# Optimization experiments

Measured on AMD Instinct MI355X. Metric: run time of the kernel, lower is better.

The kernel has to match this reference:

```python
import jax, jax.numpy as jnp
import numpy as np

K = 1024            # atoms per chain
L = 4 * K - 9       # 2*(K-3) sin/cos dihedrals + (K-2) len13 + (K-1) bond lengths
EPS = 1e-6


def _denorm(v, lo, hi):
    # map [-1, 1] -> [lo, hi]
    return (v + 1.0) * 0.5 * (hi - lo) + lo


def _output_arr2values(v):
    # split flat NN output into (sin/cos dihedrals, hedron len13, bond lengths)
    n_d = K - 3
    sc = v[: 2 * n_d].reshape(n_d, 2)                     # (sin, cos) per dihedral
    d13 = _denorm(v[2 * n_d : 2 * n_d + K - 2], 1.5, 5.0)  # 1-3 distances, [1.5, 5]
    bl = _denorm(v[2 * n_d + K - 2 :], 0.9, 3.0)           # bond lengths,  [0.9, 3]
    return sc, d13, bl


def _len2ang(sc, d13, bl):
    # bond angles via law of cosines from consecutive bond lengths + 1-3 distance
    l1, l2 = bl[:-1], bl[1:]
    ct = (l1 * l1 + l2 * l2 - d13 * d13) / (2.0 * l1 * l2)
    theta = jnp.arccos(jnp.clip(ct, -1.0 + EPS, 1.0 - EPS))   # (K-2,) radians
    chi = jnp.arctan2(sc[:, 0], sc[:, 1])                      # (K-3,) radians
    return theta, chi


def _len_ang2coords(bl, theta, chi):
    # sequential NeRF chain extension: place atom i from atoms i-3, i-2, i-1
    a0 = jnp.zeros(3, dtype=bl.dtype)
    a1 = jnp.array([1.0, 0.0, 0.0], dtype=bl.dtype) * bl[0]
    t0 = theta[0]
    a2 = a1 + bl[1] * jnp.stack([-jnp.cos(t0), jnp.sin(t0), jnp.zeros((), bl.dtype)])

    def step(carry, inp):
        a, b, c = carry
        l, th, ch = inp
        bc = c - b
        bc = bc / (jnp.linalg.norm(bc) + EPS)
        n = jnp.cross(b - a, bc)
        n = n / (jnp.linalg.norm(n) + EPS)
        m = jnp.cross(n, bc)
        st = jnp.sin(th)
        d = c + l * (-jnp.cos(th) * bc + st * jnp.cos(ch) * m + st * jnp.sin(ch) * n)
        return (b, c, d), d

    _, rest = jax.lax.scan(step, (a0, a1, a2), (bl[2:], theta[1:], chi))
    return jnp.concatenate([jnp.stack([a0, a1, a2]), rest], axis=0)  # (K, 3)


def _chain2coords(v):
    sc, d13, bl = _output_arr2values(v)
    theta, chi = _len2ang(sc, d13, bl)
    return _len_ang2coords(bl, theta, chi)


def setup_inputs() -> dict:
    key = jax.random.key(0)
    k1, k2 = jax.random.split(key)
    B = 2048
    predictions = 2.0 * jax.random.uniform(k1, (B, L), dtype=jnp.float32) - 1.0
    targets = 2.0 * jax.random.uniform(k2, (B, L), dtype=jnp.float32) - 1.0
    return {"predictions": predictions, "targets": targets}


def reference(predictions, targets):
    p = jnp.clip(predictions, -1.0, 1.0)           # only predictions are clamped
    pred_coords = jax.vmap(_chain2coords)(p)        # (B, K, 3)
    targ_coords = jax.vmap(_chain2coords)(targets)  # (B, K, 3)
    return jnp.mean(jnp.square(pred_coords - targ_coords))
```

## Files before the change

kernel.cpp:

```cpp
#include <hip/hip_runtime.h>


#define LROW  4087
#define NSTEP 1021
#define NROW  2048
#define CHUNK 16
#define EPSF  1e-6f
#define INVMEAN (1.0f / (2048.0f * 1024.0f * 3.0f))

__device__ __forceinline__ float frcp(float x){ return __builtin_amdgcn_rcpf(x); }
__device__ __forceinline__ float frsq(float x){ return __builtin_amdgcn_rsqf(x); }

template<bool CLIP>
__device__ __forceinline__ void chainScan(
    const float* __restrict__ v, const int ln, const int j0,
    float tl[CHUNK][3],
    float &g0x, float &g0y, float &g0z,
    float &g1x, float &g1y, float &g1z,
    float &g2x, float &g2y, float &g2z,
    float &gtx, float &gty, float &gtz,
    float &a1x, float &a2x, float &a2y)
{
  float rb0 = v[3064], rd0 = v[2042], rb1 = v[3065];
  if (CLIP){
    rb0 = fminf(fmaxf(rb0, -1.f), 1.f);
    rd0 = fminf(fmaxf(rd0, -1.f), 1.f);
    rb1 = fminf(fmaxf(rb1, -1.f), 1.f);
  }

  float s0[CHUNK], s1[CHUNK], dd[CHUNK], bv[CHUNK+1];
  #pragma unroll
  for (int k = 0; k < CHUNK; ++k){
    s0[k] = v[2*(j0+k)];
    s1[k] = v[2*(j0+k)+1];
    dd[k] = v[2043 + j0 + k];
  }
  #pragma unroll
  for (int m = 0; m <= CHUNK; ++m){
    int ix = 3065 + j0 + m;
    if (ix > 4086) ix = 4086;
    float b = v[ix];
    if (CLIP) b = fminf(fmaxf(b, -1.f), 1.f);
    bv[m] = fmaf(b, 1.05f, 1.95f);
  }

  float c0x,c0y,c0z, c1x,c1y,c1z, c2x,c2y,c2z, tx,ty,tz;
  #pragma unroll
  for (int k = 0; k < CHUNK; ++k){
    float a0 = s0[k], a1v = s1[k], dr = dd[k];
    if (CLIP){
      a0  = fminf(fmaxf(a0,  -1.f), 1.f);
      a1v = fminf(fmaxf(a1v, -1.f), 1.f);
      dr  = fminf(fmaxf(dr,  -1.f), 1.f);
    }
    const float d  = fmaf(dr, 1.75f, 3.25f);
    const float b1 = bv[k], b2 = bv[k+1];
    float ct = (b1*b1 + b2*b2 - d*d) * frcp(2.0f*b1*b2);
    ct = fminf(fmaxf(ct, -1.0f + EPSF), 1.0f - EPSF);
    const float omc = fmaxf(1.0f - ct*ct, 1e-12f);
    const float ist = frsq(omc);
    const float st  = omc * ist;
    const float r2 = a0*a0 + a1v*a1v;
    const bool ok = r2 > 1e-36f;
    const float ir = ok ? frsq(r2) : 0.0f;
    const float scv = a0 * ir;
    const float ccv = ok ? a1v * ir : 1.0f;
    const float hx = -ct, hy = st*ccv, hz = st*scv;
    if (k == 0){
      c0x=hx;      c0y=hy;      c0z=hz;
      c1x=-st;     c1y=hx*ccv;  c1z=hx*scv;
      c2x=0.0f;    c2y=-scv;    c2z=ccv;
      tx=b2*hx;    ty=b2*hy;    tz=b2*hz;
    } else {
      const float n0x = c0x*hx + c1x*hy + c2x*hz;
      const float n0y = c0y*hx + c1y*hy + c2y*hz;
      const float n0z = c0z*hx + c1z*hy + c2z*hz;
      tx = fmaf(b2, n0x, tx); ty = fmaf(b2, n0y, ty); tz = fmaf(b2, n0z, tz);
      const float n1x = ist * fmaf(hx, n0x, -c0x);
      const float n1y = ist * fmaf(hx, n0y, -c0y);
      const float n1z = ist * fmaf(hx, n0z, -c0z);
      const float n2x = fmaf(ccv, c2x, -scv*c1x);
      const float n2y = fmaf(ccv, c2y, -scv*c1y);
      const float n2z = fmaf(ccv, c2z, -scv*c1z);
      c0x=n0x; c0y=n0y; c0z=n0z;
      c1x=n1x; c1y=n1y; c1z=n1z;
      c2x=n2x; c2y=n2y; c2z=n2z;
    }
    tl[k][0]=tx; tl[k][1]=ty; tl[k][2]=tz;
  }

  float r0x=c0x, r0y=c0y, r0z=c0z, r1x=c1x, r1y=c1y, r1z=c1z;
  #pragma unroll
  for (int off = 1; off < 64; off <<= 1){
    const float o0x=__shfl_up(r0x,off), o0y=__shfl_up(r0y,off), o0z=__shfl_up(r0z,off);
    const float o1x=__shfl_up(r1x,off), o1y=__shfl_up(r1y,off), o1z=__shfl_up(r1z,off);
    const float o2x = o0y*o1z - o0z*o1y;
    const float o2y = o0z*o1x - o0x*o1z;
    const float o2z = o0x*o1y - o0y*o1x;
    const float n0x = o0x*r0x + o1x*r0y + o2x*r0z;
    const float n0y = o0y*r0x + o1y*r0y + o2y*r0z;
    const float n0z = o0z*r0x + o1z*r0y + o2z*r0z;
    const float n1x = o0x*r1x + o1x*r1y + o2x*r1z;
    const float n1y = o0y*r1x + o1y*r1y + o2y*r1z;
    const float n1z = o0z*r1x + o1z*r1y + o2z*r1z;
    if (ln >= off){
      r0x=n0x; r0y=n0y; r0z=n0z;
      r1x=n1x; r1y=n1y; r1z=n1z;
    }
  }

  float e0x=__shfl_up(r0x,1), e0y=__shfl_up(r0y,1), e0z=__shfl_up(r0z,1);
  float e1x=__shfl_up(r1x,1), e1y=__shfl_up(r1y,1), e1z=__shfl_up(r1z,1);
  if (ln == 0){ e0x=1.f; e0y=0.f; e0z=0.f; e1x=0.f; e1y=1.f; e1z=0.f; }

  {
    const float x2x = e0y*e1z - e0z*e1y;
    const float x2y = e0z*e1x - e0x*e1z;
    const float x2z = e0x*e1y - e0y*e1x;
    const float wx = e0x*tx + e1x*ty + x2x*tz;
    const float wy = e0y*tx + e1y*ty + x2y*tz;
    const float wz = e0z*tx + e1z*ty + x2z*tz;
    float sx=wx, sy=wy, sz=wz;
    #pragma unroll
    for (int off = 1; off < 64; off <<= 1){
      const float ax=__shfl_up(sx,off), ay=__shfl_up(sy,off), az=__shfl_up(sz,off);
      if (ln >= off){ sx+=ax; sy+=ay; sz+=az; }
    }
    tx = sx - wx; ty = sy - wy; tz = sz - wz;
  }

  const float bl0 = fmaf(rb0, 1.05f, 1.95f);
  const float d0  = fmaf(rd0, 1.75f, 3.25f);
  const float b1f = fmaf(rb1, 1.05f, 1.95f);
  float ct0 = (bl0*bl0 + b1f*b1f - d0*d0) * frcp(2.0f*bl0*b1f);
  ct0 = fminf(fmaxf(ct0, -1.0f + EPSF), 1.0f - EPSF);
  const float st0 = sqrtf(fmaxf(1.0f - ct0*ct0, 0.0f));
  a1x = bl0;
  a2x = bl0 - b1f*ct0;
  a2y = b1f*st0;

  const float e2x = e0y*e1z - e0z*e1y;
  const float e2y = e0z*e1x - e0x*e1z;
  const float e2z = e0x*e1y - e0y*e1x;

  g0x = -ct0*e0x - st0*e0y; g0y = st0*e0x - ct0*e0y; g0z = e0z;
  g1x = -ct0*e1x - st0*e1y; g1y = st0*e1x - ct0*e1y; g1z = e1z;
  g2x = -ct0*e2x - st0*e2y; g2y = st0*e2x - ct0*e2y; g2z = e2z;
  gtx = a2x - ct0*tx - st0*ty;
  gty = a2y + st0*tx - ct0*ty;
  gtz = tz;
}

__global__ void __launch_bounds__(64) __attribute__((amdgpu_waves_per_eu(2, 2)))
rmsd_kernel(const float* __restrict__ pred, const float* __restrict__ targ,
            float* __restrict__ ws){
  const int row = blockIdx.x;
  const int ln  = threadIdx.x;
  const int j0  = ln * CHUNK;

  const float* __restrict__ vp = pred + (size_t)row * LROW;
  const float* __restrict__ vt = targ + (size_t)row * LROW;

  float tlP[CHUNK][3], tlT[CHUNK][3];
  float P0x,P0y,P0z, P1x,P1y,P1z, P2x,P2y,P2z, Ptx,Pty,Ptz, Pa1,Pa2x,Pa2y;
  float T0x,T0y,T0z, T1x,T1y,T1z, T2x,T2y,T2z, Ttx,Tty,Ttz, Ta1,Ta2x,Ta2y;

  chainScan<true >(vp, ln, j0, tlP, P0x,P0y,P0z, P1x,P1y,P1z, P2x,P2y,P2z,
                   Ptx,Pty,Ptz, Pa1,Pa2x,Pa2y);
  chainScan<false>(vt, ln, j0, tlT, T0x,T0y,T0z, T1x,T1y,T1z, T2x,T2y,T2z,
                   Ttx,Tty,Ttz, Ta1,Ta2x,Ta2y);

  const float D00 = P0x*T0x + P0y*T0y + P0z*T0z;
  const float D10 = P1x*T0x + P1y*T0y + P1z*T0z;
  const float D20 = P2x*T0x + P2y*T0y + P2z*T0z;
  const float D01 = P0x*T1x + P0y*T1y + P0z*T1z;
  const float D11 = P1x*T1x + P1y*T1y + P1z*T1z;
  const float D21 = P2x*T1x + P2y*T1y + P2z*T1z;
  const float D02 = P0x*T2x + P0y*T2y + P0z*T2z;
  const float D12 = P1x*T2x + P1y*T2y + P1z*T2z;
  const float D22 = P2x*T2x + P2y*T2y + P2z*T2z;
  const float bx = Ttx - Ptx, by = Tty - Pty, bz = Ttz - Ptz;
  const float dtx = P0x*bx + P0y*by + P0z*bz;
  const float dty = P1x*bx + P1y*by + P1z*bz;
  const float dtz = P2x*bx + P2y*by + P2z*bz;

  float acc = 0.0f;
  if (ln == 0){
    const float dx = Pa1  - Ta1;
    const float dy = Pa2x - Ta2x;
    const float dz = Pa2y - Ta2y;
    acc = dx*dx + dy*dy + dz*dz;
  }
  #pragma unroll
  for (int k = 0; k < CHUNK; ++k){
    if (j0 + k < NSTEP){
      const float vx = tlT[k][0], vy = tlT[k][1], vz = tlT[k][2];
      const float wx = dtx + D00*vx + D01*vy + D02*vz;
      const float wy = dty + D10*vx + D11*vy + D12*vz;
      const float wz = dtz + D20*vx + D21*vy + D22*vz;
      const float dx = tlP[k][0] - wx;
      const float dy = tlP[k][1] - wy;
      const float dz = tlP[k][2] - wz;
      acc = fmaf(dx, dx, acc);
      acc = fmaf(dy, dy, acc);
      acc = fmaf(dz, dz, acc);
    }
  }
  #pragma unroll
  for (int off = 32; off > 0; off >>= 1) acc += __shfl_down(acc, off);
  if (ln == 0) ws[row] = acc;
}

__global__ void __launch_bounds__(256, 1)
reduce_kernel(const float* __restrict__ ws, float* __restrict__ out){
  __shared__ float wsum[4];
  const int tid = threadIdx.x;
  float a = 0.0f;
  #pragma unroll
  for (int i = 0; i < 8; ++i) a += ws[tid + (i << 8)];
  #pragma unroll
  for (int off = 32; off > 0; off >>= 1) a += __shfl_down(a, off);
  if ((tid & 63) == 0) wsum[tid >> 6] = a;
  __syncthreads();
  if (tid == 0) out[0] = (wsum[0] + wsum[1] + wsum[2] + wsum[3]) * INVMEAN;
}

extern "C" void kernel_launch(void* const* d_in, const int* in_sizes, int n_in,
                              void* d_out, int out_size, void* d_ws, size_t ws_size,
                              hipStream_t stream) {
  const float* pred = (const float*)d_in[0];
  const float* targ = (const float*)d_in[1];
  float* out = (float*)d_out;
  float* ws  = (float*)d_ws;

  rmsd_kernel<<<NROW, 64, 0, stream>>>(pred, targ, ws);
  reduce_kernel<<<1, 256, 0, stream>>>(ws, out);
}
```

Baseline: 101.1 us.

## Replace stored per-step positions with moment accumulators and interleave both chain scans

Instead of keeping 16 local positions per chain in registers and replaying them after the lane scan, each lane now accumulates a 3x3 cross-moment matrix, sums and squared norms of its local pred/target positions. The squared error is then expanded algebraically, so the rotation and translation from the wave-level scan are applied once per lane rather than per step. The pred and target chains are computed interleaved in 4-step groups with their shuffle scans fused, and the occupancy hint rises from 2 to 4 waves per EU. This lowers register pressure to allow more waves, at the risk of float cancellation in the expanded sum-of-squares form.

```diff
diff --git a/kernel.cpp b/kernel.cpp
--- a/kernel.cpp
+++ b/kernel.cpp
@@ -11,124 +11,64 @@
 __device__ __forceinline__ float frcp(float x){ return __builtin_amdgcn_rcpf(x); }
 __device__ __forceinline__ float frsq(float x){ return __builtin_amdgcn_rsqf(x); }
 
+struct Ch { float c0x,c0y,c0z, c1x,c1y,c1z, c2x,c2y,c2z, tx,ty,tz; };
+
 template<bool CLIP>
-__device__ __forceinline__ void chainScan(
-    const float* __restrict__ v, const int ln, const int j0,
-    float tl[CHUNK][3],
+__device__ __forceinline__ void stepK(Ch& X, float s0, float s1, float dr,
+                                      const float b1, const float b2,
+                                      const bool first){
+  if (CLIP){
+    s0 = fminf(fmaxf(s0, -1.f), 1.f);
+    s1 = fminf(fmaxf(s1, -1.f), 1.f);
+    dr = fminf(fmaxf(dr, -1.f), 1.f);
+  }
+  const float d = fmaf(dr, 1.75f, 3.25f);
+  float ct = (b1*b1 + b2*b2 - d*d) * frcp(2.0f*b1*b2);
+  ct = fminf(fmaxf(ct, -1.0f + EPSF), 1.0f - EPSF);
+  const float omc = fmaxf(1.0f - ct*ct, 1e-12f);
+  const float ist = frsq(omc);
+  const float st  = omc * ist;
+  const float r2 = s0*s0 + s1*s1;
+  const bool ok = r2 > 1e-36f;
+  const float ir = ok ? frsq(r2) : 0.0f;
+  const float scv = s0 * ir;
+  const float ccv = ok ? s1 * ir : 1.0f;
+  const float hx = -ct, hy = st*ccv, hz = st*scv;
+  if (first){
+    X.c0x=hx;    X.c0y=hy;      X.c0z=hz;
+    X.c1x=-st;   X.c1y=hx*ccv;  X.c1z=hx*scv;
+    X.c2x=0.f;   X.c2y=-scv;    X.c2z=ccv;
+    X.tx=b2*hx;  X.ty=b2*hy;    X.tz=b2*hz;
+  } else {
+    const float n0x = X.c0x*hx + X.c1x*hy + X.c2x*hz;
+    const float n0y = X.c0y*hx + X.c1y*hy + X.c2y*hz;
+    const float n0z = X.c0z*hx + X.c1z*hy + X.c2z*hz;
+    X.tx = fmaf(b2, n0x, X.tx);
+    X.ty = fmaf(b2, n0y, X.ty);
+    X.tz = fmaf(b2, n0z, X.tz);
+    const float n1x = ist * fmaf(hx, n0x, -X.c0x);
+    const float n1y = ist * fmaf(hx, n0y, -X.c0y);
+    const float n1z = ist * fmaf(hx, n0z, -X.c0z);
+    const float n2x = fmaf(ccv, X.c2x, -scv*X.c1x);
+    const float n2y = fmaf(ccv, X.c2y, -scv*X.c1y);
+    const float n2z = fmaf(ccv, X.c2z, -scv*X.c1z);
+    X.c0x=n0x; X.c0y=n0y; X.c0z=n0z;
+    X.c1x=n1x; X.c1y=n1y; X.c1z=n1z;
+    X.c2x=n2x; X.c2y=n2y; X.c2z=n2z;
+  }
+}
+
+__device__ __forceinline__ void foldG(
+    const float rb0, const float rd0, const float rb1,
+    const float e0x, const float e0y, const float e0z,
+    const float e1x, const float e1y, const float e1z,
+    const float tx, const float ty, const float tz,
     float &g0x, float &g0y, float &g0z,
     float &g1x, float &g1y, float &g1z,
     float &g2x, float &g2y, float &g2z,
     float &gtx, float &gty, float &gtz,
     float &a1x, float &a2x, float &a2y)
 {
-  float rb0 = v[3064], rd0 = v[2042], rb1 = v[3065];
-  if (CLIP){
-    rb0 = fminf(fmaxf(rb0, -1.f), 1.f);
-    rd0 = fminf(fmaxf(rd0, -1.f), 1.f);
-    rb1 = fminf(fmaxf(rb1, -1.f), 1.f);
-  }
-
-  float s0[CHUNK], s1[CHUNK], dd[CHUNK], bv[CHUNK+1];
-  #pragma unroll
-  for (int k = 0; k < CHUNK; ++k){
-    s0[k] = v[2*(j0+k)];
-    s1[k] = v[2*(j0+k)+1];
-    dd[k] = v[2043 + j0 + k];
-  }
-  #pragma unroll
-  for (int m = 0; m <= CHUNK; ++m){
-    int ix = 3065 + j0 + m;
-    if (ix > 4086) ix = 4086;
-    float b = v[ix];
-    if (CLIP) b = fminf(fmaxf(b, -1.f), 1.f);
-    bv[m] = fmaf(b, 1.05f, 1.95f);
-  }
-
-  float c0x,c0y,c0z, c1x,c1y,c1z, c2x,c2y,c2z, tx,ty,tz;
-  #pragma unroll
-  for (int k = 0; k < CHUNK; ++k){
-    float a0 = s0[k], a1v = s1[k], dr = dd[k];
-    if (CLIP){
-      a0  = fminf(fmaxf(a0,  -1.f), 1.f);
-      a1v = fminf(fmaxf(a1v, -1.f), 1.f);
-      dr  = fminf(fmaxf(dr,  -1.f), 1.f);
-    }
-    const float d  = fmaf(dr, 1.75f, 3.25f);
-    const float b1 = bv[k], b2 = bv[k+1];
-    float ct = (b1*b1 + b2*b2 - d*d) * frcp(2.0f*b1*b2);
-    ct = fminf(fmaxf(ct, -1.0f + EPSF), 1.0f - EPSF);
-    const float omc = fmaxf(1.0f - ct*ct, 1e-12f);
-    const float ist = frsq(omc);
-    const float st  = omc * ist;
-    const float r2 = a0*a0 + a1v*a1v;
-    const bool ok = r2 > 1e-36f;
-    const float ir = ok ? frsq(r2) : 0.0f;
-    const float scv = a0 * ir;
-    const float ccv = ok ? a1v * ir : 1.0f;
-    const float hx = -ct, hy = st*ccv, hz = st*scv;
-    if (k == 0){
-      c0x=hx;      c0y=hy;      c0z=hz;
-      c1x=-st;     c1y=hx*ccv;  c1z=hx*scv;
-      c2x=0.0f;    c2y=-scv;    c2z=ccv;
-      tx=b2*hx;    ty=b2*hy;    tz=b2*hz;
-    } else {
-      const float n0x = c0x*hx + c1x*hy + c2x*hz;
-      const float n0y = c0y*hx + c1y*hy + c2y*hz;
-      const float n0z = c0z*hx + c1z*hy + c2z*hz;
-      tx = fmaf(b2, n0x, tx); ty = fmaf(b2, n0y, ty); tz = fmaf(b2, n0z, tz);
-      const float n1x = ist * fmaf(hx, n0x, -c0x);
-      const float n1y = ist * fmaf(hx, n0y, -c0y);
-      const float n1z = ist * fmaf(hx, n0z, -c0z);
-      const float n2x = fmaf(ccv, c2x, -scv*c1x);
-      const float n2y = fmaf(ccv, c2y, -scv*c1y);
-      const float n2z = fmaf(ccv, c2z, -scv*c1z);
-      c0x=n0x; c0y=n0y; c0z=n0z;
-      c1x=n1x; c1y=n1y; c1z=n1z;
-      c2x=n2x; c2y=n2y; c2z=n2z;
-    }
-    tl[k][0]=tx; tl[k][1]=ty; tl[k][2]=tz;
-  }
-
-  float r0x=c0x, r0y=c0y, r0z=c0z, r1x=c1x, r1y=c1y, r1z=c1z;
-  #pragma unroll
-  for (int off = 1; off < 64; off <<= 1){
-    const float o0x=__shfl_up(r0x,off), o0y=__shfl_up(r0y,off), o0z=__shfl_up(r0z,off);
-    const float o1x=__shfl_up(r1x,off), o1y=__shfl_up(r1y,off), o1z=__shfl_up(r1z,off);
-    const float o2x = o0y*o1z - o0z*o1y;
-    const float o2y = o0z*o1x - o0x*o1z;
-    const float o2z = o0x*o1y - o0y*o1x;
-    const float n0x = o0x*r0x + o1x*r0y + o2x*r0z;
-    const float n0y = o0y*r0x + o1y*r0y + o2y*r0z;
-    const float n0z = o0z*r0x + o1z*r0y + o2z*r0z;
-    const float n1x = o0x*r1x + o1x*r1y + o2x*r1z;
-    const float n1y = o0y*r1x + o1y*r1y + o2y*r1z;
-    const float n1z = o0z*r1x + o1z*r1y + o2z*r1z;
-    if (ln >= off){
-      r0x=n0x; r0y=n0y; r0z=n0z;
-      r1x=n1x; r1y=n1y; r1z=n1z;
-    }
-  }
-
-  float e0x=__shfl_up(r0x,1), e0y=__shfl_up(r0y,1), e0z=__shfl_up(r0z,1);
-  float e1x=__shfl_up(r1x,1), e1y=__shfl_up(r1y,1), e1z=__shfl_up(r1z,1);
-  if (ln == 0){ e0x=1.f; e0y=0.f; e0z=0.f; e1x=0.f; e1y=1.f; e1z=0.f; }
-
-  {
-    const float x2x = e0y*e1z - e0z*e1y;
-    const float x2y = e0z*e1x - e0x*e1z;
-    const float x2z = e0x*e1y - e0y*e1x;
-    const float wx = e0x*tx + e1x*ty + x2x*tz;
-    const float wy = e0y*tx + e1y*ty + x2y*tz;
-    const float wz = e0z*tx + e1z*ty + x2z*tz;
-    float sx=wx, sy=wy, sz=wz;
-    #pragma unroll
-    for (int off = 1; off < 64; off <<= 1){
-      const float ax=__shfl_up(sx,off), ay=__shfl_up(sy,off), az=__shfl_up(sz,off);
-      if (ln >= off){ sx+=ax; sy+=ay; sz+=az; }
-    }
-    tx = sx - wx; ty = sy - wy; tz = sz - wz;
-  }
-
   const float bl0 = fmaf(rb0, 1.05f, 1.95f);
   const float d0  = fmaf(rd0, 1.75f, 3.25f);
   const float b1f = fmaf(rb1, 1.05f, 1.95f);
@@ -138,11 +78,9 @@
   a1x = bl0;
   a2x = bl0 - b1f*ct0;
   a2y = b1f*st0;
-
   const float e2x = e0y*e1z - e0z*e1y;
   const float e2y = e0z*e1x - e0x*e1z;
   const float e2z = e0x*e1y - e0y*e1x;
-
   g0x = -ct0*e0x - st0*e0y; g0y = st0*e0x - ct0*e0y; g0z = e0z;
   g1x = -ct0*e1x - st0*e1y; g1y = st0*e1x - ct0*e1y; g1z = e1z;
   g2x = -ct0*e2x - st0*e2y; g2y = st0*e2x - ct0*e2y; g2z = e2z;
@@ -151,7 +89,7 @@
   gtz = tz;
 }
 
-__global__ void __launch_bounds__(64) __attribute__((amdgpu_waves_per_eu(2, 2)))
+__global__ void __launch_bounds__(64) __attribute__((amdgpu_waves_per_eu(4, 4)))
 rmsd_kernel(const float* __restrict__ pred, const float* __restrict__ targ,
             float* __restrict__ ws){
   const int row = blockIdx.x;
@@ -161,14 +99,127 @@
   const float* __restrict__ vp = pred + (size_t)row * LROW;
   const float* __restrict__ vt = targ + (size_t)row * LROW;
 
-  float tlP[CHUNK][3], tlT[CHUNK][3];
+  Ch P, T;
+  float C00=0,C01=0,C02=0, C10=0,C11=0,C12=0, C20=0,C21=0,C22=0;
+  float sux=0,suy=0,suz=0, svx=0,svy=0,svz=0, suu=0, svv=0;
+
+  #pragma unroll
+  for (int h = 0; h < 4; ++h){
+    const int base = j0 + (h << 2);
+    float pS0[4], pS1[4], pDD[4], pBV[5];
+    float tS0[4], tS1[4], tDD[4], tBV[5];
+    #pragma unroll
+    for (int k = 0; k < 4; ++k){
+      pS0[k] = vp[2*(base+k)];   pS1[k] = vp[2*(base+k)+1];
+      tS0[k] = vt[2*(base+k)];   tS1[k] = vt[2*(base+k)+1];
+      pDD[k] = vp[2043 + base + k];
+      tDD[k] = vt[2043 + base + k];
+    }
+    #pragma unroll
+    for (int m = 0; m < 5; ++m){
+      int ix = 3065 + base + m;
+      if (ix > 4086) ix = 4086;
+      float bp = vp[ix];
+      bp = fminf(fmaxf(bp, -1.f), 1.f);
+      pBV[m] = fmaf(bp, 1.05f, 1.95f);
+      tBV[m] = fmaf(vt[ix], 1.05f, 1.95f);
+    }
+    #pragma unroll
+    for (int k = 0; k < 4; ++k){
+      const bool first = (h == 0) && (k == 0);
+      stepK<true >(P, pS0[k], pS1[k], pDD[k], pBV[k], pBV[k+1], first);
+      stepK<false>(T, tS0[k], tS1[k], tDD[k], tBV[k], tBV[k+1], first);
+      if (base + k < NSTEP){
+        const float ux=P.tx, uy=P.ty, uz=P.tz;
+        const float vx=T.tx, vy=T.ty, vz=T.tz;
+        C00=fmaf(ux,vx,C00); C01=fmaf(ux,vy,C01); C02=fmaf(ux,vz,C02);
+        C10=fmaf(uy,vx,C10); C11=fmaf(uy,vy,C11); C12=fmaf(uy,vz,C12);
+        C20=fmaf(uz,vx,C20); C21=fmaf(uz,vy,C21); C22=fmaf(uz,vz,C22);
+        sux+=ux; suy+=uy; suz+=uz;
+        svx+=vx; svy+=vy; svz+=vz;
+        suu=fmaf(ux,ux,suu); suu=fmaf(uy,uy,suu); suu=fmaf(uz,uz,suu);
+        svv=fmaf(vx,vx,svv); svv=fmaf(vy,vy,svv); svv=fmaf(vz,vz,svv);
+      }
+    }
+  }
+
+  float p0x=P.c0x,p0y=P.c0y,p0z=P.c0z, p1x=P.c1x,p1y=P.c1y,p1z=P.c1z;
+  float q0x=T.c0x,q0y=T.c0y,q0z=T.c0z, q1x=T.c1x,q1y=T.c1y,q1z=T.c1z;
+  #pragma unroll
+  for (int off = 1; off < 64; off <<= 1){
+    const float A0x=__shfl_up(p0x,off), A0y=__shfl_up(p0y,off), A0z=__shfl_up(p0z,off);
+    const float A1x=__shfl_up(p1x,off), A1y=__shfl_up(p1y,off), A1z=__shfl_up(p1z,off);
+    const float B0x=__shfl_up(q0x,off), B0y=__shfl_up(q0y,off), B0z=__shfl_up(q0z,off);
+    const float B1x=__shfl_up(q1x,off), B1y=__shfl_up(q1y,off), B1z=__shfl_up(q1z,off);
+    const float A2x = A0y*A1z - A0z*A1y;
+    const float A2y = A0z*A1x - A0x*A1z;
+    const float A2z = A0x*A1y - A0y*A1x;
+    const float B2x = B0y*B1z - B0z*B1y;
+    const float B2y = B0z*B1x - B0x*B1z;
+    const float B2z = B0x*B1y - B0y*B1x;
+    const float np0x = A0x*p0x + A1x*p0y + A2x*p0z;
+    const float np0y = A0y*p0x + A1y*p0y + A2y*p0z;
+    const float np0z = A0z*p0x + A1z*p0y + A2z*p0z;
+    const float np1x = A0x*p1x + A1x*p1y + A2x*p1z;
+    const float np1y = A0y*p1x + A1y*p1y + A2y*p1z;
+    const float np1z = A0z*p1x + A1z*p1y + A2z*p1z;
+    const float nq0x = B0x*q0x + B1x*q0y + B2x*q0z;
+    const float nq0y = B0y*q0x + B1y*q0y + B2y*q0z;
+    const float nq0z = B0z*q0x + B1z*q0y + B2z*q0z;
+    const float nq1x = B0x*q1x + B1x*q1y + B2x*q1z;
+    const float nq1y = B0y*q1x + B1y*q1y + B2y*q1z;
+    const float nq1z = B0z*q1x + B1z*q1y + B2z*q1z;
+    if (ln >= off){
+      p0x=np0x; p0y=np0y; p0z=np0z; p1x=np1x; p1y=np1y; p1z=np1z;
+      q0x=nq0x; q0y=nq0y; q0z=nq0z; q1x=nq1x; q1y=nq1y; q1z=nq1z;
+    }
+  }
+
+  float e0x=__shfl_up(p0x,1), e0y=__shfl_up(p0y,1), e0z=__shfl_up(p0z,1);
+  float e1x=__shfl_up(p1x,1), e1y=__shfl_up(p1y,1), e1z=__shfl_up(p1z,1);
+  float f0x=__shfl_up(q0x,1), f0y=__shfl_up(q0y,1), f0z=__shfl_up(q0z,1);
+  float f1x=__shfl_up(q1x,1), f1y=__shfl_up(q1y,1), f1z=__shfl_up(q1z,1);
+  if (ln == 0){
+    e0x=1.f; e0y=0.f; e0z=0.f; e1x=0.f; e1y=1.f; e1z=0.f;
+    f0x=1.f; f0y=0.f; f0z=0.f; f1x=0.f; f1y=1.f; f1z=0.f;
+  }
+
+  float tPx, tPy, tPz, tTx, tTy, tTz;
+  {
+    const float e2x = e0y*e1z - e0z*e1y;
+    const float e2y = e0z*e1x - e0x*e1z;
+    const float e2z = e0x*e1y - e0y*e1x;
+    const float f2x = f0y*f1z - f0z*f1y;
+    const float f2y = f0z*f1x - f0x*f1z;
+    const float f2z = f0x*f1y - f0y*f1x;
+    const float wPx = e0x*P.tx + e1x*P.ty + e2x*P.tz;
+    const float wPy = e0y*P.tx + e1y*P.ty + e2y*P.tz;
+    const float wPz = e0z*P.tx + e1z*P.ty + e2z*P.tz;
+    const float wTx = f0x*T.tx + f1x*T.ty + f2x*T.tz;
+    const float wTy = f0y*T.tx + f1y*T.ty + f2y*T.tz;
+    const float wTz = f0z*T.tx + f1z*T.ty + f2z*T.tz;
+    float sPx=wPx, sPy=wPy, sPz=wPz, sTx=wTx, sTy=wTy, sTz=wTz;
+    #pragma unroll
+    for (int off = 1; off < 64; off <<= 1){
+      const float aPx=__shfl_up(sPx,off), aPy=__shfl_up(sPy,off), aPz=__shfl_up(sPz,off);
+      const float aTx=__shfl_up(sTx,off), aTy=__shfl_up(sTy,off), aTz=__shfl_up(sTz,off);
+      if (ln >= off){ sPx+=aPx; sPy+=aPy; sPz+=aPz; sTx+=aTx; sTy+=aTy; sTz+=aTz; }
+    }
+    tPx = sPx - wPx; tPy = sPy - wPy; tPz = sPz - wPz;
+    tTx = sTx - wTx; tTy = sTy - wTy; tTz = sTz - wTz;
+  }
+
   float P0x,P0y,P0z, P1x,P1y,P1z, P2x,P2y,P2z, Ptx,Pty,Ptz, Pa1,Pa2x,Pa2y;
   float T0x,T0y,T0z, T1x,T1y,T1z, T2x,T2y,T2z, Ttx,Tty,Ttz, Ta1,Ta2x,Ta2y;
-
-  chainScan<true >(vp, ln, j0, tlP, P0x,P0y,P0z, P1x,P1y,P1z, P2x,P2y,P2z,
-                   Ptx,Pty,Ptz, Pa1,Pa2x,Pa2y);
-  chainScan<false>(vt, ln, j0, tlT, T0x,T0y,T0z, T1x,T1y,T1z, T2x,T2y,T2z,
-                   Ttx,Tty,Ttz, Ta1,Ta2x,Ta2y);
+  {
+    float rb0 = fminf(fmaxf(vp[3064], -1.f), 1.f);
+    float rd0 = fminf(fmaxf(vp[2042], -1.f), 1.f);
+    float rb1 = fminf(fmaxf(vp[3065], -1.f), 1.f);
+    foldG(rb0, rd0, rb1, e0x,e0y,e0z, e1x,e1y,e1z, tPx,tPy,tPz,
+          P0x,P0y,P0z, P1x,P1y,P1z, P2x,P2y,P2z, Ptx,Pty,Ptz, Pa1,Pa2x,Pa2y);
+    foldG(vt[3064], vt[2042], vt[3065], f0x,f0y,f0z, f1x,f1y,f1z, tTx,tTy,tTz,
+          T0x,T0y,T0z, T1x,T1y,T1z, T2x,T2y,T2z, Ttx,Tty,Ttz, Ta1,Ta2x,Ta2y);
+  }
 
   const float D00 = P0x*T0x + P0y*T0y + P0z*T0z;
   const float D10 = P1x*T0x + P1y*T0y + P1z*T0z;
@@ -184,27 +235,23 @@
   const float dty = P1x*bx + P1y*by + P1z*bz;
   const float dtz = P2x*bx + P2y*by + P2z*bz;
 
-  float acc = 0.0f;
+  const int n = (NSTEP - j0) < CHUNK ? (NSTEP - j0) : CHUNK;
+  const float Dsvx = D00*svx + D01*svy + D02*svz;
+  const float Dsvy = D10*svx + D11*svy + D12*svz;
+  const float Dsvz = D20*svx + D21*svy + D22*svz;
+  const float DC = D00*C00 + D01*C01 + D02*C02
+                 + D10*C10 + D11*C11 + D12*C12
+                 + D20*C20 + D21*C21 + D22*C22;
+  const float dd2 = dtx*dtx + dty*dty + dtz*dtz;
+  const float dDsv = dtx*Dsvx + dty*Dsvy + dtz*Dsvz;
+  const float sud  = sux*dtx + suy*dty + suz*dtz;
+  float acc = suu + svv + (float)n*dd2 + 2.0f*dDsv - 2.0f*DC - 2.0f*sud;
+
   if (ln == 0){
     const float dx = Pa1  - Ta1;
     const float dy = Pa2x - Ta2x;
     const float dz = Pa2y - Ta2y;
-    acc = dx*dx + dy*dy + dz*dz;
-  }
-  #pragma unroll
-  for (int k = 0; k < CHUNK; ++k){
-    if (j0 + k < NSTEP){
-      const float vx = tlT[k][0], vy = tlT[k][1], vz = tlT[k][2];
-      const float wx = dtx + D00*vx + D01*vy + D02*vz;
-      const float wy = dty + D10*vx + D11*vy + D12*vz;
-      const float wz = dtz + D20*vx + D21*vy + D22*vz;
-      const float dx = tlP[k][0] - wx;
-      const float dy = tlP[k][1] - wy;
-      const float dz = tlP[k][2] - wz;
-      acc = fmaf(dx, dx, acc);
-      acc = fmaf(dy, dy, acc);
-      acc = fmaf(dz, dz, acc);
-    }
+    acc += dx*dx + dy*dy + dz*dz;
   }
   #pragma unroll
   for (int off = 32; off > 0; off >>= 1) acc += __shfl_down(acc, off);
```

After: 123.1 us. +21.7%, slower.
